# Kernel optimization log

Hardware: AMD Instinct MI355X
Metric: run time of the kernel (lower is better)

Reference implementation:

```python
import jax, jax.numpy as jnp
import numpy as np
import math

D_MODEL = 256
N_HEADS = 8
HEAD_DIM = D_MODEL // N_HEADS  # 32
N_LEVELS = 4
N_POINTS = 4
SHAPES = [(112, 112), (56, 56), (28, 28), (14, 14)]
LEN_IN = sum(h * w for h, w in SHAPES)  # 16660
BATCH = 1
LEN_Q = LEN_IN


def _grid_init_bias():
    # Faithful to MSDeformAttn._reset_parameters: directional grid init for sampling_offsets bias.
    thetas = np.arange(N_HEADS, dtype=np.float32) * (2.0 * math.pi / N_HEADS)
    grid = np.stack([np.cos(thetas), np.sin(thetas)], -1)
    grid = grid / np.abs(grid).max(-1, keepdims=True)
    grid = np.tile(grid[:, None, None, :], (1, N_LEVELS, N_POINTS, 1)).copy()
    for i in range(N_POINTS):
        grid[:, :, i, :] *= i + 1
    return jnp.asarray(grid.reshape(-1), dtype=jnp.float32)


def setup_inputs() -> dict:
    key = jax.random.key(0)
    ks = jax.random.split(key, 10)
    s = 1.0 / math.sqrt(D_MODEL)
    return {
        "query": jax.random.normal(ks[0], (BATCH, LEN_Q, D_MODEL), jnp.float32),
        "reference_points": jax.random.uniform(ks[1], (BATCH, LEN_Q, N_LEVELS, 2), jnp.float32),
        "input_flatten": jax.random.normal(ks[2], (BATCH, LEN_IN, D_MODEL), jnp.float32),
        "spatial_shapes": jnp.asarray(SHAPES, dtype=jnp.int32),
        "level_start_index": jnp.asarray(np.cumsum([0] + [h * w for h, w in SHAPES])[:-1], dtype=jnp.int32),
        "W_q": jax.random.normal(ks[3], (D_MODEL, D_MODEL), jnp.float32) * s,
        "b_q": jnp.zeros((D_MODEL,), jnp.float32),
        "W_k": jax.random.normal(ks[4], (D_MODEL, D_MODEL), jnp.float32) * s,
        "b_k": jnp.zeros((D_MODEL,), jnp.float32),
        "W_v": jax.random.normal(ks[5], (D_MODEL, D_MODEL), jnp.float32) * s,
        "b_v": jnp.zeros((D_MODEL,), jnp.float32),
        "W_o": jax.random.normal(ks[6], (D_MODEL, D_MODEL), jnp.float32) * s,
        "b_o": jnp.zeros((D_MODEL,), jnp.float32),
        "W_off": jax.random.normal(ks[7], (D_MODEL, N_HEADS * N_LEVELS * N_POINTS * 2), jnp.float32) * 0.01,
        "b_off": _grid_init_bias(),
    }


def _bilinear_sample(img, grid, H, W):
    # img: (B, H*W, D) flattened feature map; grid: (B, Q, P, 2) in [-1, 1] (x, y order).
    # Matches F.grid_sample(mode='bilinear', padding_mode='zeros', align_corners=False).
    B, Q, P, _ = grid.shape
    x = ((grid[..., 0] + 1.0) * W - 1.0) * 0.5
    y = ((grid[..., 1] + 1.0) * H - 1.0) * 0.5
    x0 = jnp.floor(x)
    y0 = jnp.floor(y)
    lx = x - x0
    ly = y - y0
    x0i = x0.astype(jnp.int32)
    y0i = y0.astype(jnp.int32)

    def gather(yi, xi, w):
        valid = (xi >= 0) & (xi < W) & (yi >= 0) & (yi < H)
        idx = jnp.clip(yi, 0, H - 1) * W + jnp.clip(xi, 0, W - 1)
        v = jnp.take_along_axis(img, idx.reshape(B, Q * P, 1), axis=1)
        return v.reshape(B, Q, P, -1) * (w * valid)[..., None]

    return (gather(y0i, x0i, (1.0 - ly) * (1.0 - lx))
            + gather(y0i, x0i + 1, (1.0 - ly) * lx)
            + gather(y0i + 1, x0i, ly * (1.0 - lx))
            + gather(y0i + 1, x0i + 1, ly * lx))


def reference(query, reference_points, input_flatten, spatial_shapes, level_start_index,
              W_q, b_q, W_k, b_k, W_v, b_v, W_o, b_o, W_off, b_off):
    N, Lq, C = query.shape
    M, D, L, P = N_HEADS, HEAD_DIM, N_LEVELS, N_POINTS

    q = query @ W_q + b_q                                   # (N, Lq, C)
    value = (input_flatten @ W_v + b_v).reshape(N, -1, M, D)
    key_h = (input_flatten @ W_k + b_k).reshape(N, -1, M, D)

    offsets = (q @ W_off + b_off).reshape(N, Lq, M, L, P, 2)
    # offset_normalizer = (W_l, H_l) per level
    norm = jnp.stack([spatial_shapes[:, 1], spatial_shapes[:, 0]], -1).astype(q.dtype)
    loc = reference_points[:, :, None, :, None, :] + offsets / norm[None, None, None, :, None, :]
    grids = 2.0 * loc - 1.0                                  # (N, Lq, M, L, P, 2)

    samp_v, samp_k = [], []
    start = 0
    for lid, (H, W) in enumerate(SHAPES):
        end = start + H * W
        v_l = value[:, start:end].transpose(0, 2, 1, 3).reshape(N * M, H * W, D)
        k_l = key_h[:, start:end].transpose(0, 2, 1, 3).reshape(N * M, H * W, D)
        g_l = grids[:, :, :, lid].transpose(0, 2, 1, 3, 4).reshape(N * M, Lq, P, 2)
        samp_v.append(_bilinear_sample(v_l, g_l, H, W))      # (N*M, Lq, P, D)
        samp_k.append(_bilinear_sample(k_l, g_l, H, W))
        start = end

    v_s = jnp.stack(samp_v, axis=2).reshape(N, M, Lq, L, P, D)
    k_s = jnp.stack(samp_k, axis=2).reshape(N, M, Lq, L, P, D)

    qh = q.reshape(N, Lq, M, D)
    logits = jnp.einsum('nqmd,nmqlpd->nmqlp', qh, k_s) / math.sqrt(D)
    attn = jax.nn.softmax(logits.reshape(N, M, Lq, L * P), axis=-1).reshape(N, M, Lq, L, P)

    out = jnp.einsum('nmqlp,nmqlpd->nqmd', attn, v_s).reshape(N, Lq, C)
    return out @ W_o + b_o
```

## Files before the change

kernel.cpp:

```cpp
#include <hip/hip_runtime.h>
#include <hip/hip_bf16.h>
#include <math.h>

#define LEN_IN   16660
#define D_MODEL  256
#define N_HEADS  8

typedef __attribute__((ext_vector_type(8))) short short8v;
typedef __attribute__((ext_vector_type(4))) float f32x4;
typedef _Float16 f16x2 __attribute__((ext_vector_type(2)));
typedef _Float16 f16x8 __attribute__((ext_vector_type(8)));

__device__ __forceinline__ unsigned short f2h(float f) {
  union { unsigned short u; _Float16 h; } c;
  c.h = (_Float16)f;
  return c.u;
}
__device__ __forceinline__ float h2f(unsigned short u) {
  union { unsigned short u; _Float16 h; } c;
  c.u = u;
  return (float)c.h;
}
__device__ __forceinline__ f16x2 u2h(unsigned u) {
  union { unsigned u; f16x2 h; } c;
  c.u = u;
  return c.h;
}

__global__ __launch_bounds__(256) void cvt16(
    const float* __restrict__ a, const float* __restrict__ b,
    unsigned short* __restrict__ a16, unsigned short* __restrict__ b16) {
  const int nq = (LEN_IN * D_MODEL) / 4;
  int i = blockIdx.x * 256 + threadIdx.x;
  int stride = gridDim.x * 256;
  for (int qd = i; qd < nq; qd += stride) {
    float4 va = ((const float4*)a)[qd];
    ushort4 ha = {f2h(va.x), f2h(va.y), f2h(va.z), f2h(va.w)};
    ((ushort4*)a16)[qd] = ha;
    float4 vb = ((const float4*)b)[qd];
    ushort4 hb = {f2h(vb.x), f2h(vb.y), f2h(vb.z), f2h(vb.w)};
    ((ushort4*)b16)[qd] = hb;
  }
}

__global__ __launch_bounds__(256) void prep_B(
    const float* __restrict__ Wq, const float* __restrict__ Wk,
    const float* __restrict__ Wv, const float* __restrict__ Woff,
    const float* __restrict__ Wo,
    const float* __restrict__ bq, const float* __restrict__ boff,
    unsigned short* __restrict__ Btq, unsigned short* __restrict__ Btk,
    unsigned short* __restrict__ Btv, unsigned short* __restrict__ Btoff,
    unsigned short* __restrict__ Bto, float* __restrict__ bqo) {
  int b = blockIdx.x;
  int tid = threadIdx.x;
  if (b == 80) {
    float s = boff[tid];
    for (int i = 0; i < 256; i++) s += bq[i] * Woff[(size_t)i * 256 + tid];
    bqo[tid] = s;
    return;
  }
  __shared__ float tile[64][65];
  int mat = b >> 4, t = b & 15;
  int ti = t >> 2, tj = t & 3;
  const float* W = (mat == 0) ? Wq : (mat == 1) ? Wk : (mat == 2) ? Wv
                 : (mat == 3) ? Woff : Wo;
  unsigned short* Bt = (mat == 0) ? Btq : (mat == 1) ? Btk : (mat == 2) ? Btv
                     : (mat == 3) ? Btoff : Bto;
  #pragma unroll
  for (int i = 0; i < 16; i++) {
    int idx = tid + i * 256;
    int kr = idx >> 6, nc = idx & 63;
    tile[kr][nc] = W[(size_t)(ti * 64 + kr) * 256 + tj * 64 + nc];
  }
  __syncthreads();
  #pragma unroll
  for (int i = 0; i < 16; i++) {
    int idx = tid + i * 256;
    int nr = idx >> 6, kc = idx & 63;
    Bt[(size_t)(tj * 64 + nr) * 256 + ti * 64 + kc] = f2h(tile[kc][nr]);
  }
}

__global__ __launch_bounds__(256) void gemm_wqo(
    const float* __restrict__ Wq, const unsigned short* __restrict__ Btoff,
    unsigned short* __restrict__ Btqo) {
  const int P = 40;
  __shared__ short As[64 * P], Bs[64 * P];
  int tid = threadIdx.x;
  int m0 = blockIdx.x * 64, n0 = blockIdx.y * 64;
  int w = tid >> 6, l = tid & 63;
  int r = l & 15, g = l >> 4;
  int mi = (w >> 1) * 32, ni = (w & 1) * 32;
  int sm = tid >> 2, sp = tid & 3;

  f32x4 acc[2][2];
  #pragma unroll
  for (int a = 0; a < 2; a++)
    #pragma unroll
    for (int b = 0; b < 2; b++) acc[a][b] = (f32x4){0.f, 0.f, 0.f, 0.f};

  for (int k0 = 0; k0 < 256; k0 += 32) {
    const float* src = Wq + (size_t)(m0 + sm) * 256 + k0 + sp * 8;
    float4 u0 = *(const float4*)src;
    float4 u1 = *(const float4*)(src + 4);
    f16x8 hv = {(_Float16)u0.x, (_Float16)u0.y, (_Float16)u0.z, (_Float16)u0.w,
                (_Float16)u1.x, (_Float16)u1.y, (_Float16)u1.z, (_Float16)u1.w};
    *(f16x8*)&As[sm * P + sp * 8] = hv;
    *(short8v*)&Bs[sm * P + sp * 8] =
        *(const short8v*)&Btoff[(size_t)(n0 + sm) * 256 + k0 + sp * 8];
    __syncthreads();
    f16x8 af[2], bf[2];
    #pragma unroll
    for (int a = 0; a < 2; a++)
      af[a] = *(f16x8*)&As[(mi + a * 16 + r) * P + g * 8];
    #pragma unroll
    for (int b = 0; b < 2; b++)
      bf[b] = *(f16x8*)&Bs[(ni + b * 16 + r) * P + g * 8];
    #pragma unroll
    for (int a = 0; a < 2; a++)
      #pragma unroll
      for (int b = 0; b < 2; b++)
        acc[a][b] = __builtin_amdgcn_mfma_f32_16x16x32_f16(af[a], bf[b], acc[a][b], 0, 0, 0);
    __syncthreads();
  }
  #pragma unroll
  for (int a = 0; a < 2; a++)
    #pragma unroll
    for (int b = 0; b < 2; b++) {
      int col = n0 + ni + b * 16 + r;
      #pragma unroll
      for (int i = 0; i < 4; i++) {
        int row = m0 + mi + a * 16 + g * 4 + i;
        Btqo[(size_t)col * 256 + row] = f2h(acc[a][b][i]);
      }
    }
}

__global__ __launch_bounds__(256) void gemm_qkv(
    const unsigned short* __restrict__ q16, const unsigned short* __restrict__ in16,
    const unsigned short* __restrict__ Btq,
    const unsigned short* __restrict__ Btk,
    const unsigned short* __restrict__ Btv,
    const unsigned short* __restrict__ Btqo,
    const float* __restrict__ bq, const float* __restrict__ bk,
    const float* __restrict__ bv, const float* __restrict__ bqo,
    unsigned short* __restrict__ qp_out, unsigned* __restrict__ kv_out,
    unsigned short* __restrict__ offs_out, int M) {
  const int P = 72;
  __shared__ short As[128 * P], B1[64 * P], B2[64 * P];
  int z = blockIdx.z;
  const unsigned short* A = (z == 1) ? in16 : q16;
  const unsigned short* Bt1 = (z == 0) ? Btq : (z == 1) ? Btk : Btqo;
  int tid = threadIdx.x;
  int m0 = blockIdx.x * 128, n0 = blockIdx.y * 64;
  int w = tid >> 6, l = tid & 63;
  int r = l & 15, g = l >> 4;
  int mi = (w >> 1) * 64, ni = (w & 1) * 32;
  int arow = tid >> 1, ach = (tid & 1) * 32;
  int brow = tid >> 2, bch = (tid & 3) * 16;

  f32x4 acc1[4][2], acc2[4][2];
  #pragma unroll
  for (int a = 0; a < 4; a++)
    #pragma unroll
    for (int b = 0; b < 2; b++) {
      acc1[a][b] = (f32x4){0.f, 0.f, 0.f, 0.f};
      acc2[a][b] = (f32x4){0.f, 0.f, 0.f, 0.f};
    }

  for (int k0 = 0; k0 < 256; k0 += 64) {
    int gm = m0 + arow;
    short8v a0 = {0,0,0,0,0,0,0,0}, a1 = a0, a2 = a0, a3 = a0;
    if (gm < M) {
      const unsigned short* src = A + (size_t)gm * 256 + k0 + ach;
      a0 = *(const short8v*)src;
      a1 = *(const short8v*)(src + 8);
      a2 = *(const short8v*)(src + 16);
      a3 = *(const short8v*)(src + 24);
    }
    *(short8v*)&As[arow * P + ach] = a0;
    *(short8v*)&As[arow * P + ach + 8] = a1;
    *(short8v*)&As[arow * P + ach + 16] = a2;
    *(short8v*)&As[arow * P + ach + 24] = a3;
    {
      const unsigned short* bsrc = Bt1 + (size_t)(n0 + brow) * 256 + k0 + bch;
      *(short8v*)&B1[brow * P + bch] = *(const short8v*)bsrc;
      *(short8v*)&B1[brow * P + bch + 8] = *(const short8v*)(bsrc + 8);
    }
    if (z == 1) {
      const unsigned short* bsrc = Btv + (size_t)(n0 + brow) * 256 + k0 + bch;
      *(short8v*)&B2[brow * P + bch] = *(const short8v*)bsrc;
      *(short8v*)&B2[brow * P + bch + 8] = *(const short8v*)(bsrc + 8);
    }
    __syncthreads();

    f16x8 af[4][2], b1f[2][2], b2f[2][2];
    #pragma unroll
    for (int a = 0; a < 4; a++)
      #pragma unroll
      for (int ks = 0; ks < 2; ks++)
        af[a][ks] = *(f16x8*)&As[(mi + a * 16 + r) * P + ks * 32 + g * 8];
    #pragma unroll
    for (int b = 0; b < 2; b++)
      #pragma unroll
      for (int ks = 0; ks < 2; ks++)
        b1f[b][ks] = *(f16x8*)&B1[(ni + b * 16 + r) * P + ks * 32 + g * 8];
    if (z == 1) {
      #pragma unroll
      for (int b = 0; b < 2; b++)
        #pragma unroll
        for (int ks = 0; ks < 2; ks++)
          b2f[b][ks] = *(f16x8*)&B2[(ni + b * 16 + r) * P + ks * 32 + g * 8];
    }
    #pragma unroll
    for (int a = 0; a < 4; a++)
      #pragma unroll
      for (int b = 0; b < 2; b++)
        #pragma unroll
        for (int ks = 0; ks < 2; ks++) {
          acc1[a][b] = __builtin_amdgcn_mfma_f32_16x16x32_f16(af[a][ks], b1f[b][ks], acc1[a][b], 0, 0, 0);
          if (z == 1)
            acc2[a][b] = __builtin_amdgcn_mfma_f32_16x16x32_f16(af[a][ks], b2f[b][ks], acc2[a][b], 0, 0, 0);
        }
    __syncthreads();
  }

  #pragma unroll
  for (int a = 0; a < 4; a++)
    #pragma unroll
    for (int b = 0; b < 2; b++) {
      int col = n0 + ni + b * 16 + r;
      if (z == 0) {
        float bc = bq[col];
        #pragma unroll
        for (int i = 0; i < 4; i++) {
          int row = m0 + mi + a * 16 + g * 4 + i;
          if (row < M) qp_out[(size_t)row * 256 + col] = f2h(acc1[a][b][i] + bc);
        }
      } else if (z == 1) {
        float bkc = bk[col], bvc = bv[col];
        int hh = col >> 5, cc = col & 31;
        #pragma unroll
        for (int i = 0; i < 4; i++) {
          int row = m0 + mi + a * 16 + g * 4 + i;
          if (row < M) {
            unsigned kh = f2h(acc1[a][b][i] + bkc);
            unsigned vh = f2h(acc2[a][b][i] + bvc);
            kv_out[((size_t)hh * LEN_IN + row) * 32 + cc] = kh | (vh << 16);
          }
        }
      } else {
        float bc = bqo[col];
        #pragma unroll
        for (int i = 0; i < 4; i++) {
          int row = m0 + mi + a * 16 + g * 4 + i;
          if (row < M) offs_out[(size_t)row * 256 + col] = f2h(acc1[a][b][i] + bc);
        }
      }
    }
}

__global__ __launch_bounds__(256) void gemm_out(
    const unsigned short* __restrict__ A,
    const unsigned short* __restrict__ Bt,
    const float* __restrict__ bias, float* __restrict__ C, int M) {
  const int P = 72;
  __shared__ short As[128 * P], Bs[64 * P];
  int tid = threadIdx.x;
  int m0 = blockIdx.x * 128, n0 = blockIdx.y * 64;
  int w = tid >> 6, l = tid & 63;
  int r = l & 15, g = l >> 4;
  int mi = (w >> 1) * 64, ni = (w & 1) * 32;
  int arow = tid >> 1, ach = (tid & 1) * 32;
  int brow = tid >> 2, bch = (tid & 3) * 16;

  f32x4 acc[4][2];
  #pragma unroll
  for (int a = 0; a < 4; a++)
    #pragma unroll
    for (int b = 0; b < 2; b++) acc[a][b] = (f32x4){0.f, 0.f, 0.f, 0.f};

  for (int k0 = 0; k0 < 256; k0 += 64) {
    int gm = m0 + arow;
    short8v a0 = {0,0,0,0,0,0,0,0}, a1 = a0, a2 = a0, a3 = a0;
    if (gm < M) {
      const unsigned short* src = A + (size_t)gm * 256 + k0 + ach;
      a0 = *(const short8v*)src;
      a1 = *(const short8v*)(src + 8);
      a2 = *(const short8v*)(src + 16);
      a3 = *(const short8v*)(src + 24);
    }
    *(short8v*)&As[arow * P + ach] = a0;
    *(short8v*)&As[arow * P + ach + 8] = a1;
    *(short8v*)&As[arow * P + ach + 16] = a2;
    *(short8v*)&As[arow * P + ach + 24] = a3;
    const unsigned short* bsrc = Bt + (size_t)(n0 + brow) * 256 + k0 + bch;
    *(short8v*)&Bs[brow * P + bch] = *(const short8v*)bsrc;
    *(short8v*)&Bs[brow * P + bch + 8] = *(const short8v*)(bsrc + 8);
    __syncthreads();

    f16x8 af[4][2], bf[2][2];
    #pragma unroll
    for (int a = 0; a < 4; a++)
      #pragma unroll
      for (int ks = 0; ks < 2; ks++)
        af[a][ks] = *(f16x8*)&As[(mi + a * 16 + r) * P + ks * 32 + g * 8];
    #pragma unroll
    for (int b = 0; b < 2; b++)
      #pragma unroll
      for (int ks = 0; ks < 2; ks++)
        bf[b][ks] = *(f16x8*)&Bs[(ni + b * 16 + r) * P + ks * 32 + g * 8];
    #pragma unroll
    for (int a = 0; a < 4; a++)
      #pragma unroll
      for (int b = 0; b < 2; b++)
        #pragma unroll
        for (int ks = 0; ks < 2; ks++)
          acc[a][b] = __builtin_amdgcn_mfma_f32_16x16x32_f16(af[a][ks], bf[b][ks], acc[a][b], 0, 0, 0);
    __syncthreads();
  }
  #pragma unroll
  for (int a = 0; a < 4; a++)
    #pragma unroll
    for (int b = 0; b < 2; b++) {
      int col = n0 + ni + b * 16 + r;
      float bc = bias[col];
      #pragma unroll
      for (int i = 0; i < 4; i++) {
        int row = m0 + mi + a * 16 + g * 4 + i;
        if (row < M) C[(size_t)row * 256 + col] = acc[a][b][i] + bc;
      }
    }
}

__global__ __launch_bounds__(256) void sample_attn(
    const unsigned short* __restrict__ qp,
    const unsigned short* __restrict__ offs,
    const float* __restrict__ rp,
    const unsigned* __restrict__ kv,
    unsigned short* __restrict__ attn_out) {
  __shared__ float lbuf[4][16];
  __shared__ float ebuf[4][16];
  __shared__ float vbuf[4][16][36];

  int tid = threadIdx.x;
  int wslot = tid >> 6;
  int lane = tid & 63;
  int wid = blockIdx.x * 4 + wslot;
  int q = wid >> 3;
  int h = wid & 7;

  int pt = lane >> 2;
  int c8 = (lane & 3) * 8;
  int l5 = lane & 31;

  float offv = h2f(offs[(size_t)q * 256 + h * 32 + l5]);
  float rpv = (l5 < 8) ? rp[(size_t)q * 8 + l5] : 0.f;

  int l = pt >> 2, pp = pt & 3;
  int W = 112 >> l;
  int start = (int)((50176u - (50176u >> (2 * l))) / 3u);

  float off_x = __shfl(offv, l * 8 + pp * 2 + 0, 32);
  float off_y = __shfl(offv, l * 8 + pp * 2 + 1, 32);
  float rp_x = __shfl(rpv, l * 2 + 0, 32);
  float rp_y = __shfl(rpv, l * 2 + 1, 32);

  float x = rp_x * (float)W + off_x - 0.5f;
  float y = rp_y * (float)W + off_y - 0.5f;
  float x0f = floorf(x), y0f = floorf(y);
  float lx = x - x0f, ly = y - y0f;
  int x0 = (int)x0f, y0 = (int)y0f;
  float wx0 = 1.f - lx, wy0 = 1.f - ly;
  float tw[4] = {wy0 * wx0, wy0 * lx, ly * wx0, ly * lx};

  const unsigned* kvh = kv + (size_t)h * LEN_IN * 32 + c8;

  f16x2 acc[8];
  #pragma unroll
  for (int j = 0; j < 8; j++) acc[j] = (f16x2){(_Float16)0.f, (_Float16)0.f};

  #pragma unroll
  for (int tap = 0; tap < 4; tap++) {
    int yy = y0 + (tap >> 1), xx = x0 + (tap & 1);
    bool valid = ((unsigned)xx < (unsigned)W) & ((unsigned)yy < (unsigned)W);
    float wgt = valid ? tw[tap] : 0.f;
    int pix = valid ? (start + yy * W + xx) : start;
    const unsigned* p = kvh + (size_t)pix * 32;
    uint4 u0 = *(const uint4*)p;
    uint4 u1 = *(const uint4*)(p + 4);
    _Float16 wh = (_Float16)wgt;
    f16x2 w2 = {wh, wh};
    acc[0] += w2 * u2h(u0.x);
    acc[1] += w2 * u2h(u0.y);
    acc[2] += w2 * u2h(u0.z);
    acc[3] += w2 * u2h(u0.w);
    acc[4] += w2 * u2h(u1.x);
    acc[5] += w2 * u2h(u1.y);
    acc[6] += w2 * u2h(u1.z);
    acc[7] += w2 * u2h(u1.w);
  }

  uint4 qa = *(const uint4*)(qp + (size_t)q * 256 + h * 32 + c8);
  float dot = 0.f;
  f16x2 kp;
  kp[0] = acc[0][0]; kp[1] = acc[1][0];
  dot = __builtin_amdgcn_fdot2(u2h(qa.x), kp, dot, false);
  kp[0] = acc[2][0]; kp[1] = acc[3][0];
  dot = __builtin_amdgcn_fdot2(u2h(qa.y), kp, dot, false);
  kp[0] = acc[4][0]; kp[1] = acc[5][0];
  dot = __builtin_amdgcn_fdot2(u2h(qa.z), kp, dot, false);
  kp[0] = acc[6][0]; kp[1] = acc[7][0];
  dot = __builtin_amdgcn_fdot2(u2h(qa.w), kp, dot, false);
  dot += __shfl_xor(dot, 1, 64);
  dot += __shfl_xor(dot, 2, 64);
  if ((lane & 3) == 0) lbuf[wslot][pt] = dot * 0.17677669529663687f;

  float4 v0 = {(float)acc[0][1], (float)acc[1][1], (float)acc[2][1], (float)acc[3][1]};
  float4 v1 = {(float)acc[4][1], (float)acc[5][1], (float)acc[6][1], (float)acc[7][1]};
  *(float4*)&vbuf[wslot][pt][c8] = v0;
  *(float4*)&vbuf[wslot][pt][c8 + 4] = v1;
  __syncthreads();

  float lg = lbuf[wslot][lane & 15];
  float m = lg;
  m = fmaxf(m, __shfl_xor(m, 1, 64));
  m = fmaxf(m, __shfl_xor(m, 2, 64));
  m = fmaxf(m, __shfl_xor(m, 4, 64));
  m = fmaxf(m, __shfl_xor(m, 8, 64));
  float e = __expf(lg - m);
  float s = e;
  s += __shfl_xor(s, 1, 64);
  s += __shfl_xor(s, 2, 64);
  s += __shfl_xor(s, 4, 64);
  s += __shfl_xor(s, 8, 64);
  if (lane < 16) ebuf[wslot][lane] = e;
  float inv = 1.f / s;
  __syncthreads();

  if (lane < 32) {
    float o = 0.f;
    #pragma unroll
    for (int p = 0; p < 16; p++) o += ebuf[wslot][p] * vbuf[wslot][p][lane];
    attn_out[(size_t)q * 256 + h * 32 + lane] = f2h(o * inv);
  }
}

extern "C" void kernel_launch(void* const* d_in, const int* in_sizes, int n_in,
                              void* d_out, int out_size, void* d_ws, size_t ws_size,
                              hipStream_t stream) {
  const float* query = (const float*)d_in[0];
  const float* rp    = (const float*)d_in[1];
  const float* inp   = (const float*)d_in[2];
  const float* W_q   = (const float*)d_in[5];
  const float* b_q   = (const float*)d_in[6];
  const float* W_k   = (const float*)d_in[7];
  const float* b_k   = (const float*)d_in[8];
  const float* W_v   = (const float*)d_in[9];
  const float* b_v   = (const float*)d_in[10];
  const float* W_o   = (const float*)d_in[11];
  const float* b_o   = (const float*)d_in[12];
  const float* W_off = (const float*)d_in[13];
  const float* b_off = (const float*)d_in[14];
  float* out = (float*)d_out;

  const size_t nelem = (size_t)LEN_IN * D_MODEL;
  unsigned short* q16   = (unsigned short*)d_ws;
  unsigned short* in16  = q16 + nelem;
  unsigned short* qp    = in16 + nelem;
  unsigned short* offsb = qp + nelem;
  unsigned short* attn  = offsb + nelem;
  unsigned* kvp = (unsigned*)(attn + nelem);
  unsigned short* Btq   = (unsigned short*)(kvp + nelem);
  unsigned short* Btk   = Btq + 256 * 256;
  unsigned short* Btv   = Btk + 256 * 256;
  unsigned short* Btoff = Btv + 256 * 256;
  unsigned short* Bto   = Btoff + 256 * 256;
  unsigned short* Btqo  = Bto + 256 * 256;
  float* bqo = (float*)(Btqo + 256 * 256);

  dim3 blk(256);
  dim3 ggrid((LEN_IN + 127) / 128, D_MODEL / 64);
  dim3 ggrid3((LEN_IN + 127) / 128, D_MODEL / 64, 3);

  cvt16<<<2048, blk, 0, stream>>>(query, inp, q16, in16);
  prep_B<<<81, blk, 0, stream>>>(W_q, W_k, W_v, W_off, W_o, b_q, b_off,
                                 Btq, Btk, Btv, Btoff, Bto, bqo);
  gemm_wqo<<<dim3(4, 4), blk, 0, stream>>>(W_q, Btoff, Btqo);

  gemm_qkv<<<ggrid3, blk, 0, stream>>>(q16, in16, Btq, Btk, Btv, Btqo,
                                       b_q, b_k, b_v, bqo,
                                       qp, kvp, offsb, LEN_IN);

  int n_blocks = LEN_IN * N_HEADS / 4;
  sample_attn<<<n_blocks, blk, 0, stream>>>(qp, offsb, rp, kvp, attn);

  gemm_out<<<ggrid, blk, 0, stream>>>(attn, Bto, b_o, out, LEN_IN);
}
```

Baseline: 131.3 us.

## Fuse prep kernels into one launch and drop max-subtraction in softmax

Merges the fp16 conversion, weight transpose, and W_q·W_off precompute into one kernel. The W_off operand is now transposed and converted inside the small GEMM instead of coming from an intermediate buffer, which removes two launches and the serialization between them. In sample_attn the softmax no longer subtracts the max, and it folds normalization into the value weights before the LDS write, removing one barrier and two shared buffers. Skipping the max subtraction risks overflow if logits grow large.

```diff
diff --git a/kernel.cpp b/kernel.cpp
--- a/kernel.cpp
+++ b/kernel.cpp
@@ -27,113 +27,129 @@
   return c.h;
 }
 
-__global__ __launch_bounds__(256) void cvt16(
-    const float* __restrict__ a, const float* __restrict__ b,
-    unsigned short* __restrict__ a16, unsigned short* __restrict__ b16) {
-  const int nq = (LEN_IN * D_MODEL) / 4;
-  int i = blockIdx.x * 256 + threadIdx.x;
-  int stride = gridDim.x * 256;
-  for (int qd = i; qd < nq; qd += stride) {
-    float4 va = ((const float4*)a)[qd];
-    ushort4 ha = {f2h(va.x), f2h(va.y), f2h(va.z), f2h(va.w)};
-    ((ushort4*)a16)[qd] = ha;
-    float4 vb = ((const float4*)b)[qd];
-    ushort4 hb = {f2h(vb.x), f2h(vb.y), f2h(vb.z), f2h(vb.w)};
-    ((ushort4*)b16)[qd] = hb;
-  }
-}
-
-__global__ __launch_bounds__(256) void prep_B(
+__global__ __launch_bounds__(256) void mega_prep(
+    const float* __restrict__ query, const float* __restrict__ inp,
     const float* __restrict__ Wq, const float* __restrict__ Wk,
     const float* __restrict__ Wv, const float* __restrict__ Woff,
     const float* __restrict__ Wo,
     const float* __restrict__ bq, const float* __restrict__ boff,
+    unsigned short* __restrict__ q16, unsigned short* __restrict__ in16,
     unsigned short* __restrict__ Btq, unsigned short* __restrict__ Btk,
-    unsigned short* __restrict__ Btv, unsigned short* __restrict__ Btoff,
-    unsigned short* __restrict__ Bto, float* __restrict__ bqo) {
+    unsigned short* __restrict__ Btv, unsigned short* __restrict__ Bto,
+    unsigned short* __restrict__ Btqo, float* __restrict__ bqo) {
   int b = blockIdx.x;
   int tid = threadIdx.x;
-  if (b == 80) {
+
+  if (b < 2048) {
+    const int nq = (LEN_IN * D_MODEL) / 4;
+    int i = b * 256 + tid;
+    const int stride = 2048 * 256;
+    for (int qd = i; qd < nq; qd += stride) {
+      float4 va = ((const float4*)query)[qd];
+      ushort4 ha = {f2h(va.x), f2h(va.y), f2h(va.z), f2h(va.w)};
+      ((ushort4*)q16)[qd] = ha;
+      float4 vb = ((const float4*)inp)[qd];
+      ushort4 hb = {f2h(vb.x), f2h(vb.y), f2h(vb.z), f2h(vb.w)};
+      ((ushort4*)in16)[qd] = hb;
+    }
+    return;
+  }
+
+  if (b < 2128) {
+    __shared__ float tile[64][65];
+    int bb = b - 2048;
+    int mat = bb >> 4, t = bb & 15;
+    int ti = t >> 2, tj = t & 3;
+    const float* W = (mat == 0) ? Wq : (mat == 1) ? Wk : (mat == 2) ? Wv
+                   : (mat == 3) ? Woff : Wo;
+    unsigned short* Bt = (mat == 0) ? Btq : (mat == 1) ? Btk : (mat == 2) ? Btv
+                       : (mat == 3) ? nullptr : Bto;
+    if (mat == 3) return;
+    #pragma unroll
+    for (int i = 0; i < 16; i++) {
+      int idx = tid + i * 256;
+      int kr = idx >> 6, nc = idx & 63;
+      tile[kr][nc] = W[(size_t)(ti * 64 + kr) * 256 + tj * 64 + nc];
+    }
+    __syncthreads();
+    #pragma unroll
+    for (int i = 0; i < 16; i++) {
+      int idx = tid + i * 256;
+      int nr = idx >> 6, kc = idx & 63;
+      Bt[(size_t)(tj * 64 + nr) * 256 + ti * 64 + kc] = f2h(tile[kc][nr]);
+    }
+    return;
+  }
+
+  if (b == 2128) {
     float s = boff[tid];
     for (int i = 0; i < 256; i++) s += bq[i] * Woff[(size_t)i * 256 + tid];
     bqo[tid] = s;
     return;
   }
-  __shared__ float tile[64][65];
-  int mat = b >> 4, t = b & 15;
-  int ti = t >> 2, tj = t & 3;
-  const float* W = (mat == 0) ? Wq : (mat == 1) ? Wk : (mat == 2) ? Wv
-                 : (mat == 3) ? Woff : Wo;
-  unsigned short* Bt = (mat == 0) ? Btq : (mat == 1) ? Btk : (mat == 2) ? Btv
-                     : (mat == 3) ? Btoff : Bto;
-  #pragma unroll
-  for (int i = 0; i < 16; i++) {
-    int idx = tid + i * 256;
-    int kr = idx >> 6, nc = idx & 63;
-    tile[kr][nc] = W[(size_t)(ti * 64 + kr) * 256 + tj * 64 + nc];
-  }
-  __syncthreads();
-  #pragma unroll
-  for (int i = 0; i < 16; i++) {
-    int idx = tid + i * 256;
-    int nr = idx >> 6, kc = idx & 63;
-    Bt[(size_t)(tj * 64 + nr) * 256 + ti * 64 + kc] = f2h(tile[kc][nr]);
-  }
-}
-
-__global__ __launch_bounds__(256) void gemm_wqo(
-    const float* __restrict__ Wq, const unsigned short* __restrict__ Btoff,
-    unsigned short* __restrict__ Btqo) {
-  const int P = 40;
-  __shared__ short As[64 * P], Bs[64 * P];
-  int tid = threadIdx.x;
-  int m0 = blockIdx.x * 64, n0 = blockIdx.y * 64;
-  int w = tid >> 6, l = tid & 63;
-  int r = l & 15, g = l >> 4;
-  int mi = (w >> 1) * 32, ni = (w & 1) * 32;
-  int sm = tid >> 2, sp = tid & 3;
-
-  f32x4 acc[2][2];
-  #pragma unroll
-  for (int a = 0; a < 2; a++)
-    #pragma unroll
-    for (int b = 0; b < 2; b++) acc[a][b] = (f32x4){0.f, 0.f, 0.f, 0.f};
-
-  for (int k0 = 0; k0 < 256; k0 += 32) {
-    const float* src = Wq + (size_t)(m0 + sm) * 256 + k0 + sp * 8;
-    float4 u0 = *(const float4*)src;
-    float4 u1 = *(const float4*)(src + 4);
-    f16x8 hv = {(_Float16)u0.x, (_Float16)u0.y, (_Float16)u0.z, (_Float16)u0.w,
-                (_Float16)u1.x, (_Float16)u1.y, (_Float16)u1.z, (_Float16)u1.w};
-    *(f16x8*)&As[sm * P + sp * 8] = hv;
-    *(short8v*)&Bs[sm * P + sp * 8] =
-        *(const short8v*)&Btoff[(size_t)(n0 + sm) * 256 + k0 + sp * 8];
-    __syncthreads();
-    f16x8 af[2], bf[2];
+
+  {
+    const int P = 40;
+    __shared__ short As[64 * P], Bs[64 * P];
+    int t = b - 2129;
+    int m0 = (t >> 2) * 64, n0 = (t & 3) * 64;
+    int w = tid >> 6, l = tid & 63;
+    int r = l & 15, g = l >> 4;
+    int mi = (w >> 1) * 32, ni = (w & 1) * 32;
+    int sm = tid >> 2, sp = tid & 3;
+    int kr = tid >> 3, nc = (tid & 7) * 8;
+
+    f32x4 acc[2][2];
     #pragma unroll
     for (int a = 0; a < 2; a++)
-      af[a] = *(f16x8*)&As[(mi + a * 16 + r) * P + g * 8];
-    #pragma unroll
-    for (int b = 0; b < 2; b++)
-      bf[b] = *(f16x8*)&Bs[(ni + b * 16 + r) * P + g * 8];
+      #pragma unroll
+      for (int c = 0; c < 2; c++) acc[a][c] = (f32x4){0.f, 0.f, 0.f, 0.f};
+
+    for (int k0 = 0; k0 < 256; k0 += 32) {
+      const float* src = Wq + (size_t)(m0 + sm) * 256 + k0 + sp * 8;
+      float4 u0 = *(const float4*)src;
+      float4 u1 = *(const float4*)(src + 4);
+      f16x8 hv = {(_Float16)u0.x, (_Float16)u0.y, (_Float16)u0.z, (_Float16)u0.w,
+                  (_Float16)u1.x, (_Float16)u1.y, (_Float16)u1.z, (_Float16)u1.w};
+      *(f16x8*)&As[sm * P + sp * 8] = hv;
+      const float* wsrc = Woff + (size_t)(k0 + kr) * 256 + n0 + nc;
+      float4 w0 = *(const float4*)wsrc;
+      float4 w1 = *(const float4*)(wsrc + 4);
+      Bs[(nc + 0) * P + kr] = (short)f2h(w0.x);
+      Bs[(nc + 1) * P + kr] = (short)f2h(w0.y);
+      Bs[(nc + 2) * P + kr] = (short)f2h(w0.z);
+      Bs[(nc + 3) * P + kr] = (short)f2h(w0.w);
+      Bs[(nc + 4) * P + kr] = (short)f2h(w1.x);
+      Bs[(nc + 5) * P + kr] = (short)f2h(w1.y);
+      Bs[(nc + 6) * P + kr] = (short)f2h(w1.z);
+      Bs[(nc + 7) * P + kr] = (short)f2h(w1.w);
+      __syncthreads();
+      f16x8 af[2], bf[2];
+      #pragma unroll
+      for (int a = 0; a < 2; a++)
+        af[a] = *(f16x8*)&As[(mi + a * 16 + r) * P + g * 8];
+      #pragma unroll
+      for (int c = 0; c < 2; c++)
+        bf[c] = *(f16x8*)&Bs[(ni + c * 16 + r) * P + g * 8];
+      #pragma unroll
+      for (int a = 0; a < 2; a++)
+        #pragma unroll
+        for (int c = 0; c < 2; c++)
+          acc[a][c] = __builtin_amdgcn_mfma_f32_16x16x32_f16(af[a], bf[c], acc[a][c], 0, 0, 0);
+      __syncthreads();
+    }
     #pragma unroll
     for (int a = 0; a < 2; a++)
       #pragma unroll
-      for (int b = 0; b < 2; b++)
-        acc[a][b] = __builtin_amdgcn_mfma_f32_16x16x32_f16(af[a], bf[b], acc[a][b], 0, 0, 0);
-    __syncthreads();
-  }
-  #pragma unroll
-  for (int a = 0; a < 2; a++)
-    #pragma unroll
-    for (int b = 0; b < 2; b++) {
-      int col = n0 + ni + b * 16 + r;
-      #pragma unroll
-      for (int i = 0; i < 4; i++) {
-        int row = m0 + mi + a * 16 + g * 4 + i;
-        Btqo[(size_t)col * 256 + row] = f2h(acc[a][b][i]);
+      for (int c = 0; c < 2; c++) {
+        int col = n0 + ni + c * 16 + r;
+        #pragma unroll
+        for (int i = 0; i < 4; i++) {
+          int row = m0 + mi + a * 16 + g * 4 + i;
+          Btqo[(size_t)col * 256 + row] = f2h(acc[a][c][i]);
+        }
       }
-    }
+  }
 }
 
 __global__ __launch_bounds__(256) void gemm_qkv(
@@ -339,8 +355,6 @@
     const float* __restrict__ rp,
     const unsigned* __restrict__ kv,
     unsigned short* __restrict__ attn_out) {
-  __shared__ float lbuf[4][16];
-  __shared__ float ebuf[4][16];
   __shared__ float vbuf[4][16][36];
 
   int tid = threadIdx.x;
@@ -414,35 +428,28 @@
   dot = __builtin_amdgcn_fdot2(u2h(qa.w), kp, dot, false);
   dot += __shfl_xor(dot, 1, 64);
   dot += __shfl_xor(dot, 2, 64);
-  if ((lane & 3) == 0) lbuf[wslot][pt] = dot * 0.17677669529663687f;
-
-  float4 v0 = {(float)acc[0][1], (float)acc[1][1], (float)acc[2][1], (float)acc[3][1]};
-  float4 v1 = {(float)acc[4][1], (float)acc[5][1], (float)acc[6][1], (float)acc[7][1]};
+
+  float e = __expf(dot * 0.17677669529663687f);
+  float s = e;
+  s += __shfl_xor(s, 4, 64);
+  s += __shfl_xor(s, 8, 64);
+  s += __shfl_xor(s, 16, 64);
+  s += __shfl_xor(s, 32, 64);
+  float wsc = e / s;
+
+  float4 v0 = {wsc * (float)acc[0][1], wsc * (float)acc[1][1],
+               wsc * (float)acc[2][1], wsc * (float)acc[3][1]};
+  float4 v1 = {wsc * (float)acc[4][1], wsc * (float)acc[5][1],
+               wsc * (float)acc[6][1], wsc * (float)acc[7][1]};
   *(float4*)&vbuf[wslot][pt][c8] = v0;
   *(float4*)&vbuf[wslot][pt][c8 + 4] = v1;
   __syncthreads();
 
-  float lg = lbuf[wslot][lane & 15];
-  float m = lg;
-  m = fmaxf(m, __shfl_xor(m, 1, 64));
-  m = fmaxf(m, __shfl_xor(m, 2, 64));
-  m = fmaxf(m, __shfl_xor(m, 4, 64));
-  m = fmaxf(m, __shfl_xor(m, 8, 64));
-  float e = __expf(lg - m);
-  float s = e;
-  s += __shfl_xor(s, 1, 64);
-  s += __shfl_xor(s, 2, 64);
-  s += __shfl_xor(s, 4, 64);
-  s += __shfl_xor(s, 8, 64);
-  if (lane < 16) ebuf[wslot][lane] = e;
-  float inv = 1.f / s;
-  __syncthreads();
-
   if (lane < 32) {
     float o = 0.f;
     #pragma unroll
-    for (int p = 0; p < 16; p++) o += ebuf[wslot][p] * vbuf[wslot][p][lane];
-    attn_out[(size_t)q * 256 + h * 32 + lane] = f2h(o * inv);
+    for (int p = 0; p < 16; p++) o += vbuf[wslot][p][lane];
+    attn_out[(size_t)q * 256 + h * 32 + lane] = f2h(o);
   }
 }
 
@@ -474,8 +481,7 @@
   unsigned short* Btq   = (unsigned short*)(kvp + nelem);
   unsigned short* Btk   = Btq + 256 * 256;
   unsigned short* Btv   = Btk + 256 * 256;
-  unsigned short* Btoff = Btv + 256 * 256;
-  unsigned short* Bto   = Btoff + 256 * 256;
+  unsigned short* Bto   = Btv + 256 * 256;
   unsigned short* Btqo  = Bto + 256 * 256;
   float* bqo = (float*)(Btqo + 256 * 256);
 
@@ -483,10 +489,9 @@
   dim3 ggrid((LEN_IN + 127) / 128, D_MODEL / 64);
   dim3 ggrid3((LEN_IN + 127) / 128, D_MODEL / 64, 3);
 
-  cvt16<<<2048, blk, 0, stream>>>(query, inp, q16, in16);
-  prep_B<<<81, blk, 0, stream>>>(W_q, W_k, W_v, W_off, W_o, b_q, b_off,
-                                 Btq, Btk, Btv, Btoff, Bto, bqo);
-  gemm_wqo<<<dim3(4, 4), blk, 0, stream>>>(W_q, Btoff, Btqo);
+  mega_prep<<<2145, blk, 0, stream>>>(query, inp, W_q, W_k, W_v, W_off, W_o,
+                                      b_q, b_off, q16, in16,
+                                      Btq, Btk, Btv, Bto, Btqo, bqo);
 
   gemm_qkv<<<ggrid3, blk, 0, stream>>>(q16, in16, Btq, Btk, Btv, Btqo,
                                        b_q, b_k, b_v, bqo,
```

Measured after the change: 119.7 us. 1.1x faster.
